# Kernel optimization log

Measured on AMD Instinct MI355X. Metric: run time of the kernel, lower is better.

Reference implementation:

```python
import jax, jax.numpy as jnp
import numpy as np
from jax import lax

P = 4
PSIZE = P * P
ITERS = 3
EPS = 1e-8
LAMBDA = 1e-3  # inverse-temperature used by the EM routing sigmoid (yl-1993 style)
LN2PI_HALF = 0.5 * float(np.log(2.0 * np.pi))


def extract_patches(x, K, stride, pad):
    """x: (b,h,w,c) -> (b,oh,ow,K*K,c) sliding-window patches."""
    if pad:
        x = jnp.pad(x, ((0, 0), (pad, pad), (pad, pad), (0, 0)))
    b, h, w, c = x.shape
    oh = (h - K) // stride + 1
    ow = (w - K) // stride + 1
    slices = []
    for ki in range(K):
        for kj in range(K):
            slices.append(x[:, ki:ki + stride * (oh - 1) + 1:stride,
                             kj:kj + stride * (ow - 1) + 1:stride, :])
    return jnp.stack(slices, axis=3)  # (b,oh,ow,K*K,c)


def em_routing(v, a_in, beta_u, beta_a, iters=ITERS):
    """EM routing (Hinton et al. 2018).
    v: (n, Bin, Cout, PSIZE) votes, a_in: (n, Bin, 1) input activations.
    Returns mu: (n, Cout, PSIZE), a_out: (n, Cout).
    """
    n, Bin, Cout, psize = v.shape
    r = jnp.full((n, Bin, Cout), 1.0 / Cout, dtype=v.dtype)
    mu = None
    a_out = None
    for it in range(iters):
        # ---- M step ----
        r_w = r * a_in                                    # (n,Bin,Cout)
        r_sum = r_w.sum(axis=1, keepdims=True)            # (n,1,Cout)
        coeff = (r_w / (r_sum + EPS))[..., None]          # (n,Bin,Cout,1)
        mu = jnp.sum(coeff * v, axis=1, keepdims=True)    # (n,1,Cout,psize)
        sigma_sq = jnp.sum(coeff * (v - mu) ** 2, axis=1, keepdims=True) + EPS
        cost_h = (beta_u[None, None, :, None] + 0.5 * jnp.log(sigma_sq)) * r_sum[..., None]
        a_out = jax.nn.sigmoid(LAMBDA * (beta_a[None, None, :] - cost_h.sum(axis=3)))  # (n,1,Cout)
        # ---- E step ----
        if it < iters - 1:
            ln_p = -(v - mu) ** 2 / (2.0 * sigma_sq) - 0.5 * jnp.log(sigma_sq) - LN2PI_HALF
            ln_ap = ln_p.sum(axis=3) + jnp.log(EPS + a_out)  # (n,Bin,Cout)
            r = jax.nn.softmax(ln_ap, axis=2)
    return mu[:, 0], a_out[:, 0]


def depthwise_caps(pose, a, W, bu, ba, K, stride):
    """DepthWiseConvCaps: each capsule type routes its own KxK spatial patch to one
    output capsule of the same type. W: (K*K, B, P, P)."""
    b = pose.shape[0]
    Bc = a.shape[-1]
    pad = K // 2
    pp = extract_patches(pose, K, stride, pad)  # (b,oh,ow,KK,B*PSIZE)
    ap = extract_patches(a, K, stride, pad)     # (b,oh,ow,KK,B)
    oh, ow = pp.shape[1], pp.shape[2]
    pm = pp.reshape(b, oh, ow, K * K, Bc, P, P)
    v = jnp.einsum('bhwkcij,kcjl->bhwkcil', pm, W)            # (b,oh,ow,KK,B,P,P)
    v = v.transpose(0, 1, 2, 4, 3, 5, 6).reshape(b * oh * ow * Bc, K * K, 1, PSIZE)
    a_in = ap.transpose(0, 1, 2, 4, 3).reshape(b * oh * ow * Bc, K * K, 1)
    mu, a_out = em_routing(v, a_in, bu, ba)
    return mu.reshape(b, oh, ow, Bc * PSIZE), a_out.reshape(b, oh, ow, Bc)


def conv_caps_1x1(pose, a, W, bu, ba):
    """ConvCaps with K=1, stride=1: per-position routing Bin -> Cout. W: (Bin,Cout,P,P)."""
    b, h, w, _ = pose.shape
    Bc, Cc = W.shape[0], W.shape[1]
    pm = pose.reshape(b * h * w, Bc, P, P)
    v = jnp.einsum('nbij,bcjl->nbcil', pm, W).reshape(b * h * w, Bc, Cc, PSIZE)
    a_in = a.reshape(b * h * w, Bc)[..., None]
    mu, a_out = em_routing(v, a_in, bu, ba)
    return mu.reshape(b, h, w, Cc * PSIZE), a_out.reshape(b, h, w, Cc)


def class_caps(pose, a, W, bu, ba):
    """Class ConvCaps: w_shared across positions + coordinate addition. W: (D,E,P,P)."""
    b, h, w, _ = pose.shape
    D, E = W.shape[0], W.shape[1]
    pm = pose.reshape(b, h, w, D, P, P)
    v = jnp.einsum('bhwdij,dejl->bhwdeil', pm, W).reshape(b, h, w, D, E, PSIZE)
    # coordinate addition on the first two vote components
    coord = jnp.zeros((h, w, PSIZE), v.dtype)
    coord = coord.at[:, :, 0].add(jnp.arange(h, dtype=v.dtype)[:, None] / h)
    coord = coord.at[:, :, 1].add(jnp.arange(w, dtype=v.dtype)[None, :] / w)
    v = v + coord[None, :, :, None, None, :]
    v = v.reshape(b, h * w * D, E, PSIZE)
    a_in = a.reshape(b, h * w * D, 1)
    mu, a_out = em_routing(v, a_in, bu, ba)
    return mu, a_out  # (b,E,PSIZE), (b,E)


def _forward(x, conv1_w, conv1_b, prim_pose_w, prim_pose_b, prim_a_w, prim_a_b,
             dw1_w, dw1_bu, dw1_ba, cc1_w, cc1_bu, cc1_ba,
             dw2_w, dw2_bu, dw2_ba, cc2_w, cc2_bu, cc2_ba,
             cls_w, cls_bu, cls_ba):
    # conv stem: k5 s2 valid
    y = lax.conv_general_dilated(x, conv1_w, (2, 2), 'VALID',
                                 dimension_numbers=('NHWC', 'HWIO', 'NHWC'))
    y = jax.nn.relu(y + conv1_b)
    # primary caps: 1x1 convs for pose and activation
    pose = jnp.einsum('bhwc,cd->bhwd', y, prim_pose_w) + prim_pose_b   # (b,h,w,B*PSIZE)
    a = jax.nn.sigmoid(jnp.einsum('bhwc,cd->bhwd', y, prim_a_w) + prim_a_b)  # (b,h,w,B)
    pose, a = depthwise_caps(pose, a, dw1_w, dw1_bu, dw1_ba, K=7, stride=2)
    pose, a = conv_caps_1x1(pose, a, cc1_w, cc1_bu, cc1_ba)
    pose, a = depthwise_caps(pose, a, dw2_w, dw2_bu, dw2_ba, K=5, stride=2)
    pose, a = conv_caps_1x1(pose, a, cc2_w, cc2_bu, cc2_ba)
    pose_cls, a_cls = class_caps(pose, a, cls_w, cls_bu, cls_ba)
    return a_cls  # (b, E)


def setup_inputs() -> dict:
    key = jax.random.key(0)
    ks = jax.random.split(key, 10)
    f32 = jnp.float32
    d = {}
    d['x'] = jax.random.normal(ks[0], (32, 64, 64, 1), f32)
    d['conv1_w'] = jax.random.normal(ks[1], (5, 5, 1, 64), f32) * 0.1
    d['conv1_b'] = jnp.zeros((64,), f32)
    d['prim_pose_w'] = jax.random.normal(ks[2], (64, 128), f32) * 0.1
    d['prim_pose_b'] = jnp.zeros((128,), f32)
    d['prim_a_w'] = jax.random.normal(ks[3], (64, 8), f32) * 0.1
    d['prim_a_b'] = jnp.zeros((8,), f32)
    d['dw1_w'] = jax.random.normal(ks[4], (49, 8, 4, 4), f32) * 0.25
    d['dw1_bu'] = jnp.zeros((1,), f32)
    d['dw1_ba'] = jnp.zeros((1,), f32)
    d['cc1_w'] = jax.random.normal(ks[5], (8, 16, 4, 4), f32) * 0.25
    d['cc1_bu'] = jnp.zeros((16,), f32)
    d['cc1_ba'] = jnp.zeros((16,), f32)
    d['dw2_w'] = jax.random.normal(ks[6], (25, 16, 4, 4), f32) * 0.25
    d['dw2_bu'] = jnp.zeros((1,), f32)
    d['dw2_ba'] = jnp.zeros((1,), f32)
    d['cc2_w'] = jax.random.normal(ks[7], (16, 16, 4, 4), f32) * 0.25
    d['cc2_bu'] = jnp.zeros((16,), f32)
    d['cc2_ba'] = jnp.zeros((16,), f32)
    d['cls_w'] = jax.random.normal(ks[8], (16, 10, 4, 4), f32) * 0.25
    d['cls_bu'] = jnp.zeros((10,), f32)
    d['cls_ba'] = jnp.zeros((10,), f32)
    return d


def reference(x, conv1_w, conv1_b, prim_pose_w, prim_pose_b, prim_a_w, prim_a_b,
              dw1_w, dw1_bu, dw1_ba, cc1_w, cc1_bu, cc1_ba,
              dw2_w, dw2_bu, dw2_ba, cc2_w, cc2_bu, cc2_ba,
              cls_w, cls_bu, cls_ba):
    return _forward(x, conv1_w, conv1_b, prim_pose_w, prim_pose_b, prim_a_w, prim_a_b,
                    dw1_w, dw1_bu, dw1_ba, cc1_w, cc1_bu, cc1_ba,
                    dw2_w, dw2_bu, dw2_ba, cc2_w, cc2_bu, cc2_ba,
                    cls_w, cls_bu, cls_ba)
```

## Files before the change

kernel.cpp:

```cpp
#include <hip/hip_runtime.h>
#include <hip/hip_bf16.h>

#define EPS 1e-8f
#define LAMBDA 1e-3f
#define LN2PI_HALF 0.9189385332046727f

__device__ __forceinline__ float sigmoidf(float x) { return 1.f / (1.f + __expf(-x)); }

__global__ __launch_bounds__(256) void stem_primary_kernel(
    const float* __restrict__ x, const float* __restrict__ w,
    const float* __restrict__ bias,
    const float* __restrict__ wp, const float* __restrict__ bp,
    const float* __restrict__ wa, const float* __restrict__ ba,
    float* __restrict__ pose, float* __restrict__ a) {
  __shared__ float wp_s[64][128];
  __shared__ float wc_s[25][64];
  __shared__ float wa_s[64][8];
  __shared__ float bias_s[64];
  __shared__ float bp_s[128];
  __shared__ float ba_s[8];
  __shared__ float xs[5][23];
  __shared__ float ys[10][64];

  int t = threadIdx.x;
  int jt = blockIdx.x % 3;
  int oi = (blockIdx.x / 3) % 30;
  int b  = blockIdx.x / 90;
  int oj0 = jt * 10;

  for (int q = t; q < 8192; q += 256) ((float*)wp_s)[q] = wp[q];
  for (int q = t; q < 1600; q += 256) ((float*)wc_s)[q] = w[q];
  for (int q = t; q < 512;  q += 256) ((float*)wa_s)[q] = wa[q];
  if (t < 64) bias_s[t] = bias[t];
  if (t < 128) bp_s[t] = bp[t];
  if (t < 8) ba_s[t] = ba[t];
  for (int q = t; q < 115; q += 256) {
    int ki = q / 23, kj = q % 23;
    xs[ki][kj] = x[(b * 64 + 2 * oi + ki) * 64 + 2 * oj0 + kj];
  }
  __syncthreads();

#pragma unroll
  for (int rep = 0; rep < 3; ++rep) {
    int q = rep * 256 + t;
    if (q < 640) {
      int pos = q >> 6, ch = q & 63;
      float s = bias_s[ch];
#pragma unroll
      for (int ki = 0; ki < 5; ++ki)
#pragma unroll
        for (int kj = 0; kj < 5; ++kj)
          s += xs[ki][2 * pos + kj] * wc_s[ki * 5 + kj][ch];
      ys[pos][ch] = fmaxf(s, 0.f);
    }
  }
  __syncthreads();

  int w_ = t >> 7, d = t & 127;
  float acc[5];
#pragma unroll
  for (int j = 0; j < 5; ++j) acc[j] = bp_s[d];
  for (int c = 0; c < 64; ++c) {
    float wv = wp_s[c][d];
#pragma unroll
    for (int j = 0; j < 5; ++j) acc[j] += ys[w_ + 2 * j][c] * wv;
  }
  size_t rowbase = (size_t)(b * 30 + oi) * 30 + oj0;
#pragma unroll
  for (int j = 0; j < 5; ++j)
    pose[(rowbase + w_ + 2 * j) * 128 + d] = acc[j];

  if (t < 80) {
    int pos = t >> 3, jj = t & 7;
    float s = ba_s[jj];
#pragma unroll 8
    for (int c = 0; c < 64; ++c) s += ys[pos][c] * wa_s[c][jj];
    a[(rowbase + pos) * 8 + jj] = sigmoidf(s);
  }
}

template <int K, int BC, int HIN, int WIN, int HOUT, int WOUT>
__global__ __launch_bounds__(256) void dw_caps_kernel(
    const float* __restrict__ pose_in, const float* __restrict__ a_in,
    const float* __restrict__ Wt,
    const float* __restrict__ bu_p, const float* __restrict__ ba_p,
    float* __restrict__ pose_out, float* __restrict__ a_out) {
  constexpr int PAD = K / 2;
  int tid = blockIdx.x * 256 + threadIdx.x;
  int p = tid & 15;
  int prob = tid >> 4;
  int c = prob % BC;
  int t1 = prob / BC;
  int oj = t1 % WOUT; t1 /= WOUT;
  int oi = t1 % HOUT;
  int b = t1 / HOUT;
  int ip = p >> 2, l = p & 3;

  int ih0 = 2 * oi - PAD, iw0 = 2 * oj - PAD;
  float rsum = 0.f, acc = 0.f, acc2 = 0.f;

  if (ih0 >= 0 && ih0 + K <= HIN && iw0 >= 0 && iw0 + K <= WIN) {
#pragma unroll
    for (int ki = 0; ki < K; ++ki) {
      int rowbase = (b * HIN + ih0 + ki) * WIN + iw0;
#pragma unroll
      for (int kj = 0; kj < K; ++kj) {
        int base = rowbase + kj;
        float ak = a_in[(size_t)base * BC + c];
        const float* pm = pose_in + ((size_t)base * BC + c) * 16 + ip * 4;
        const float* wr = Wt + ((ki * K + kj) * BC + c) * 16 + l;
        float v = pm[0] * wr[0] + pm[1] * wr[4] + pm[2] * wr[8] + pm[3] * wr[12];
        rsum += ak;
        float av = ak * v;
        acc += av;
        acc2 += av * v;
      }
    }
  } else {
#pragma unroll
    for (int ki = 0; ki < K; ++ki) {
      int ih = ih0 + ki;
      if (ih < 0 || ih >= HIN) continue;
      int rowbase = (b * HIN + ih) * WIN;
#pragma unroll
      for (int kj = 0; kj < K; ++kj) {
        int iw = iw0 + kj;
        if (iw < 0 || iw >= WIN) continue;
        int base = rowbase + iw;
        float ak = a_in[(size_t)base * BC + c];
        const float* pm = pose_in + ((size_t)base * BC + c) * 16 + ip * 4;
        const float* wr = Wt + ((ki * K + kj) * BC + c) * 16 + l;
        float v = pm[0] * wr[0] + pm[1] * wr[4] + pm[2] * wr[8] + pm[3] * wr[12];
        rsum += ak;
        float av = ak * v;
        acc += av;
        acc2 += av * v;
      }
    }
  }
  float inv = 1.f / (rsum + EPS);
  float mu = acc * inv;
  float S = rsum * inv;
  float sg = acc2 * inv - mu * mu * (2.f - S);
  sg = fmaxf(sg, 0.f) + EPS;
  float hl = 0.5f * __logf(sg);
  float ls = hl;
  ls += __shfl_xor(ls, 1, 64);
  ls += __shfl_xor(ls, 2, 64);
  ls += __shfl_xor(ls, 4, 64);
  ls += __shfl_xor(ls, 8, 64);

  size_t obase = ((size_t)(b * HOUT + oi) * WOUT + oj) * BC + c;
  pose_out[obase * 16 + p] = mu;
  if (p == 0) {
    float cost = rsum * (16.f * bu_p[0] + ls);
    a_out[obase] = sigmoidf(LAMBDA * (ba_p[0] - cost));
  }
}

template <int BIN>
__global__ __launch_bounds__(256) void cc_em_kernel(
    const float* __restrict__ pose_in, const float* __restrict__ a_arr,
    const float* __restrict__ Wt,
    const float* __restrict__ bu_p, const float* __restrict__ ba_p,
    float* __restrict__ pose_out, float* __restrict__ a_out) {
  constexpr int COUT = 16;
  __shared__ float pm_s[BIN * 16];
  __shared__ float ain_s[BIN];
  __shared__ float v_s[BIN][COUT * 16];
  __shared__ float rw_s[BIN][COUT];
  __shared__ float mu_s[COUT * 16];
  __shared__ float sg_s[COUT * 16];
  __shared__ float hl_s[COUT * 16];
  __shared__ float rsum_s[COUT];
  __shared__ float aout_s[COUT];
  __shared__ float lnap_s[BIN][COUT];

  int n = blockIdx.x, t = threadIdx.x;
  int c = t >> 4, p = t & 15;
  if (t < BIN * 16) pm_s[t] = pose_in[(size_t)n * BIN * 16 + t];
  if (t < BIN) ain_s[t] = a_arr[(size_t)n * BIN + t];
  __syncthreads();

  int ip = p >> 2, l = p & 3;
#pragma unroll
  for (int b = 0; b < BIN; ++b) {
    const float* wr = Wt + (b * COUT + c) * 16 + l;
    const float* pm = &pm_s[b * 16 + ip * 4];
    v_s[b][t] = pm[0] * wr[0] + pm[1] * wr[4] + pm[2] * wr[8] + pm[3] * wr[12];
  }
  if (t < BIN * COUT) rw_s[t / COUT][t % COUT] = (1.f / COUT) * ain_s[t / COUT];
  __syncthreads();

  for (int it = 0; it < 3; ++it) {
    if (t < COUT) {
      float s = 0.f;
#pragma unroll
      for (int b = 0; b < BIN; ++b) s += rw_s[b][t];
      rsum_s[t] = s;
    }
    __syncthreads();
    {
      float s = 0.f;
#pragma unroll
      for (int b = 0; b < BIN; ++b) s += rw_s[b][c] * v_s[b][t];
      float mu = s / (rsum_s[c] + EPS);
      mu_s[t] = mu;
      float s2 = 0.f;
#pragma unroll
      for (int b = 0; b < BIN; ++b) { float d = v_s[b][t] - mu; s2 += rw_s[b][c] * d * d; }
      float sg = s2 / (rsum_s[c] + EPS) + EPS;
      sg_s[t] = sg;
      hl_s[t] = 0.5f * __logf(sg);
    }
    __syncthreads();
    if (t < COUT) {
      float lsum = 0.f;
#pragma unroll
      for (int pp = 0; pp < 16; ++pp) lsum += hl_s[t * 16 + pp];
      float cost = rsum_s[t] * (16.f * bu_p[t] + lsum);
      aout_s[t] = sigmoidf(LAMBDA * (ba_p[t] - cost));
    }
    __syncthreads();
    if (it < 2) {
      if (t < BIN * COUT) {
        int b = t / COUT, cc = t % COUT;
        float s = __logf(EPS + aout_s[cc]) - 16.f * LN2PI_HALF;
#pragma unroll
        for (int pp = 0; pp < 16; ++pp) {
          float d = v_s[b][cc * 16 + pp] - mu_s[cc * 16 + pp];
          s += -d * d / (2.f * sg_s[cc * 16 + pp]) - hl_s[cc * 16 + pp];
        }
        lnap_s[b][cc] = s;
      }
      __syncthreads();
      if (t < BIN * COUT) {
        int b = t / COUT, cc = t % COUT;
        float m = -1e30f;
#pragma unroll
        for (int q = 0; q < COUT; ++q) m = fmaxf(m, lnap_s[b][q]);
        float Z = 0.f;
#pragma unroll
        for (int q = 0; q < COUT; ++q) Z += __expf(lnap_s[b][q] - m);
        rw_s[b][cc] = (__expf(lnap_s[b][cc] - m) / Z) * ain_s[b];
      }
      __syncthreads();
    }
  }
  pose_out[(size_t)n * COUT * 16 + t] = mu_s[t];
  if (t < COUT) a_out[(size_t)n * COUT + t] = aout_s[t];
}

__global__ __launch_bounds__(256) void cls_m_kernel(
    const float* __restrict__ pose5, const float* __restrict__ a5,
    const float* __restrict__ X, const float* __restrict__ W,
    const float* __restrict__ bu_p, const float* __restrict__ ba_p,
    float* __restrict__ mu_g, float* __restrict__ inv2_g,
    float* __restrict__ base_g, float* __restrict__ out,
    int first, int last) {
  int blk = blockIdx.x;
  int c = blk % 10, b = blk / 10;
  int t = threadIdx.x;
  int lane = t & 63, wv = t >> 6;
  const float* pg = pose5 + (size_t)b * 16384;
  __shared__ float w_s[16][16];
  {
    int d = t & 15, jj = t >> 4;
    w_s[jj][d] = W[(d * 10 + c) * 16 + jj];
  }
  __syncthreads();
  const int d = t & 15;
  float wf[16];
#pragma unroll
  for (int jj = 0; jj < 16; ++jj) wf[jj] = w_s[jj][d];

  float sA = 0.f, sV[16], sV2[16];
#pragma unroll
  for (int p = 0; p < 16; ++p) { sV[p] = 0.f; sV2[p] = 0.f; }
#pragma unroll
  for (int rep = 0; rep < 4; ++rep) {
    int bi = rep * 256 + t;
    int pos = bi >> 4;
    float rw = first ? 0.1f * a5[(size_t)b * 1024 + bi]
                     : X[(size_t)blk * 1024 + bi];
    float ci = (float)(pos >> 3) * 0.125f;
    float cj = (float)(pos & 7) * 0.125f;
    const float* pp = pg + pos * 256 + d * 16;
    float pmr[16];
#pragma unroll
    for (int q = 0; q < 16; ++q) pmr[q] = pp[q];
    sA += rw;
#pragma unroll
    for (int p = 0; p < 16; ++p) {
      int ip = p >> 2, l = p & 3;
      float v = pmr[ip * 4 + 0] * wf[0 * 4 + l] + pmr[ip * 4 + 1] * wf[1 * 4 + l]
              + pmr[ip * 4 + 2] * wf[2 * 4 + l] + pmr[ip * 4 + 3] * wf[3 * 4 + l];
      if (p == 0) v += ci;
      else if (p == 1) v += cj;
      float rv = rw * v;
      sV[p] += rv;
      sV2[p] += rv * v;
    }
  }
#pragma unroll
  for (int off = 1; off < 64; off <<= 1) {
    sA += __shfl_xor(sA, off, 64);
#pragma unroll
    for (int p = 0; p < 16; ++p) {
      sV[p]  += __shfl_xor(sV[p],  off, 64);
      sV2[p] += __shfl_xor(sV2[p], off, 64);
    }
  }
  __shared__ float red[4][36];
  if (lane == 0) {
    red[wv][0] = sA;
#pragma unroll
    for (int p = 0; p < 16; ++p) { red[wv][1 + p] = sV[p]; red[wv][17 + p] = sV2[p]; }
  }
  __syncthreads();
  if (t < 16) {
    int p = t;
    float sAf  = red[0][0] + red[1][0] + red[2][0] + red[3][0];
    float sVf  = red[0][1+p] + red[1][1+p] + red[2][1+p] + red[3][1+p];
    float sV2f = red[0][17+p] + red[1][17+p] + red[2][17+p] + red[3][17+p];
    float inv = 1.f / (sAf + EPS);
    float S = sAf * inv;
    float mu = sVf * inv;
    float sg = sV2f * inv - mu * mu * (2.f - S) + EPS;
    sg = fmaxf(sg, EPS);
    mu_g[blk * 16 + p] = mu;
    inv2_g[blk * 16 + p] = 0.5f / sg;
    float hl = 0.5f * __logf(sg);
    float lsum = hl;
    lsum += __shfl_xor(lsum, 1, 64);
    lsum += __shfl_xor(lsum, 2, 64);
    lsum += __shfl_xor(lsum, 4, 64);
    lsum += __shfl_xor(lsum, 8, 64);
    if (p == 0) {
      float cost = sAf * (16.f * bu_p[c] + lsum);
      float ao = sigmoidf(LAMBDA * (ba_p[c] - cost));
      base_g[blk] = __logf(EPS + ao) - lsum - 16.f * LN2PI_HALF;
      if (last) out[blk] = ao;
    }
  }
}

__global__ __launch_bounds__(512) void cls_e_kernel(
    const float* __restrict__ pose5, const float* __restrict__ a5,
    const float* __restrict__ W,
    const float* __restrict__ mu_g, const float* __restrict__ inv2_g,
    const float* __restrict__ base_g, float* __restrict__ X) {
  int b = blockIdx.x >> 1;
  int t = threadIdx.x;
  int bi = ((blockIdx.x & 1) << 9) + t;
  const float* pg = pose5 + (size_t)b * 16384;
  __shared__ float w2[10][16][16];
  __shared__ float mu_s[160];
  __shared__ float inv2_s[160];
  __shared__ float base_s[10];
  for (int q = t; q < 2560; q += 512) {
    int dd = q & 15, jj = (q >> 4) & 15, c = q >> 8;
    w2[c][jj][dd] = W[(dd * 10 + c) * 16 + jj];
  }
  if (t < 160) { mu_s[t] = mu_g[b * 160 + t]; inv2_s[t] = inv2_g[b * 160 + t]; }
  if (t >= 160 && t < 170) base_s[t - 160] = base_g[b * 10 + (t - 160)];
  __syncthreads();

  int pos = bi >> 4, d2 = bi & 15;
  float ci = (float)(pos >> 3) * 0.125f;
  float cj = (float)(pos & 7) * 0.125f;
  const float* pp = pg + pos * 256 + d2 * 16;
  float pmr[16];
#pragma unroll
  for (int q = 0; q < 16; ++q) pmr[q] = pp[q];
  float lnap[10];
#pragma unroll
  for (int c = 0; c < 10; ++c) {
    float wf[16];
#pragma unroll
    for (int jj = 0; jj < 16; ++jj) wf[jj] = w2[c][jj][d2];
    float s = base_s[c];
#pragma unroll
    for (int p = 0; p < 16; ++p) {
      int ip = p >> 2, l = p & 3;
      float v = pmr[ip * 4 + 0] * wf[0 * 4 + l] + pmr[ip * 4 + 1] * wf[1 * 4 + l]
              + pmr[ip * 4 + 2] * wf[2 * 4 + l] + pmr[ip * 4 + 3] * wf[3 * 4 + l];
      if (p == 0) v += ci;
      else if (p == 1) v += cj;
      float dd = v - mu_s[c * 16 + p];
      s -= dd * dd * inv2_s[c * 16 + p];
    }
    lnap[c] = s;
  }
  float m = -1e30f;
#pragma unroll
  for (int c = 0; c < 10; ++c) m = fmaxf(m, lnap[c]);
  float Z = 0.f;
  float ex[10];
#pragma unroll
  for (int c = 0; c < 10; ++c) { ex[c] = __expf(lnap[c] - m); Z += ex[c]; }
  float invZ = a5[(size_t)b * 1024 + bi] / Z;
#pragma unroll
  for (int c = 0; c < 10; ++c) X[((size_t)(b * 10 + c)) * 1024 + bi] = ex[c] * invZ;
}

extern "C" void kernel_launch(void* const* d_in, const int* in_sizes, int n_in,
                              void* d_out, int out_size, void* d_ws, size_t ws_size,
                              hipStream_t stream) {
  const float* x       = (const float*)d_in[0];
  const float* conv1_w = (const float*)d_in[1];
  const float* conv1_b = (const float*)d_in[2];
  const float* pp_w    = (const float*)d_in[3];
  const float* pp_b    = (const float*)d_in[4];
  const float* pa_w    = (const float*)d_in[5];
  const float* pa_b    = (const float*)d_in[6];
  const float* dw1_w   = (const float*)d_in[7];
  const float* dw1_bu  = (const float*)d_in[8];
  const float* dw1_ba  = (const float*)d_in[9];
  const float* cc1_w   = (const float*)d_in[10];
  const float* cc1_bu  = (const float*)d_in[11];
  const float* cc1_ba  = (const float*)d_in[12];
  const float* dw2_w   = (const float*)d_in[13];
  const float* dw2_bu  = (const float*)d_in[14];
  const float* dw2_ba  = (const float*)d_in[15];
  const float* cc2_w   = (const float*)d_in[16];
  const float* cc2_bu  = (const float*)d_in[17];
  const float* cc2_ba  = (const float*)d_in[18];
  const float* cls_w   = (const float*)d_in[19];
  const float* cls_bu  = (const float*)d_in[20];
  const float* cls_ba  = (const float*)d_in[21];
  float* out = (float*)d_out;

  float* ws = (float*)d_ws;
  float* pose1 = ws;
  float* a1    = ws + 3686400;
  float* pose2 = ws + 3916800;
  float* a2    = ws + 4838400;
  float* pose3 = ws;
  float* a3    = ws + 1843200;
  float* pose4 = ws + 1958400;
  float* a4    = ws + 2482688;
  float* pose5 = ws + 2515456;
  float* a5    = ws + 3039744;
  float* Xbuf  = ws + 3072512;
  float* mu_g  = ws + 3400192;
  float* inv2_g= ws + 3405312;
  float* base_g= ws + 3410432;

  stem_primary_kernel<<<2880, 256, 0, stream>>>(x, conv1_w, conv1_b,
                                                pp_w, pp_b, pa_w, pa_b, pose1, a1);
  dw_caps_kernel<7, 8, 30, 30, 15, 15><<<3600, 256, 0, stream>>>(
      pose1, a1, dw1_w, dw1_bu, dw1_ba, pose2, a2);
  cc_em_kernel<8><<<7200, 256, 0, stream>>>(pose2, a2, cc1_w, cc1_bu, cc1_ba, pose3, a3);
  dw_caps_kernel<5, 16, 15, 15, 8, 8><<<2048, 256, 0, stream>>>(
      pose3, a3, dw2_w, dw2_bu, dw2_ba, pose4, a4);
  cc_em_kernel<16><<<2048, 256, 0, stream>>>(pose4, a4, cc2_w, cc2_bu, cc2_ba, pose5, a5);
  cls_m_kernel<<<320, 256, 0, stream>>>(pose5, a5, Xbuf, cls_w, cls_bu, cls_ba,
                                        mu_g, inv2_g, base_g, out, 1, 0);
  cls_e_kernel<<<64, 512, 0, stream>>>(pose5, a5, cls_w, mu_g, inv2_g, base_g, Xbuf);
  cls_m_kernel<<<320, 256, 0, stream>>>(pose5, a5, Xbuf, cls_w, cls_bu, cls_ba,
                                        mu_g, inv2_g, base_g, out, 0, 0);
  cls_e_kernel<<<64, 512, 0, stream>>>(pose5, a5, cls_w, mu_g, inv2_g, base_g, Xbuf);
  cls_m_kernel<<<320, 256, 0, stream>>>(pose5, a5, Xbuf, cls_w, cls_bu, cls_ba,
                                        mu_g, inv2_g, base_g, out, 0, 1);
}
```

Measured before the change: 302.8 us.

## Stage depthwise capsule input rows and weights in shared memory per block

```diff
diff --git a/kernel.cpp b/kernel.cpp
--- a/kernel.cpp
+++ b/kernel.cpp
@@ -79,82 +79,88 @@
   }
 }
 
-template <int K, int BC, int HIN, int WIN, int HOUT, int WOUT>
+template <int K, int BC, int HIN, int WIN, int HOUT, int WOUT, int OIG, int NG>
 __global__ __launch_bounds__(256) void dw_caps_kernel(
     const float* __restrict__ pose_in, const float* __restrict__ a_in,
     const float* __restrict__ Wt,
     const float* __restrict__ bu_p, const float* __restrict__ ba_p,
     float* __restrict__ pose_out, float* __restrict__ a_out) {
   constexpr int PAD = K / 2;
-  int tid = blockIdx.x * 256 + threadIdx.x;
-  int p = tid & 15;
-  int prob = tid >> 4;
-  int c = prob % BC;
-  int t1 = prob / BC;
-  int oj = t1 % WOUT; t1 /= WOUT;
-  int oi = t1 % HOUT;
-  int b = t1 / HOUT;
-  int ip = p >> 2, l = p & 3;
-
-  int ih0 = 2 * oi - PAD, iw0 = 2 * oj - PAD;
-  float rsum = 0.f, acc = 0.f, acc2 = 0.f;
-
-  if (ih0 >= 0 && ih0 + K <= HIN && iw0 >= 0 && iw0 + K <= WIN) {
+  constexpr int RA = (2 * (OIG - 1) + K < HIN) ? (2 * (OIG - 1) + K) : HIN;
+  __shared__ float tp[RA * WIN * 20];
+  __shared__ float ta[RA * WIN];
+  __shared__ float wt[K * K * 16];
+
+  int t = threadIdx.x;
+  int g = (NG > 1) ? (blockIdx.x % NG) : 0;
+  int c = (blockIdx.x / NG) % BC;
+  int b = blockIdx.x / (NG * BC);
+  int oi_lo = g * OIG;
+  int rlo = max(0, 2 * oi_lo - PAD);
+  int rhi = min(HIN, 2 * (oi_lo + OIG - 1) - PAD + K);
+  int nrows = rhi - rlo;
+
+  for (int q = t; q < K * K * 16; q += 256) {
+    int tap = q >> 4, lj = q & 15, l = lj >> 2, j = lj & 3;
+    wt[tap * 16 + lj] = Wt[((size_t)tap * BC + c) * 16 + j * 4 + l];
+  }
+  for (int q = t; q < nrows * WIN; q += 256) {
+    int row = q / WIN, col = q % WIN;
+    ta[q] = a_in[((size_t)((b * HIN + rlo + row) * WIN + col)) * BC + c];
+  }
+  for (int q = t; q < nrows * WIN * 4; q += 256) {
+    int quad = q & 3, pc = q >> 2;
+    int row = pc / WIN, col = pc % WIN;
+    const float4 src = *(const float4*)(pose_in +
+        (((size_t)((b * HIN + rlo + row) * WIN + col)) * BC + c) * 16 + quad * 4);
+    *(float4*)(tp + (row * WIN + col) * 20 + quad * 4) = src;
+  }
+  __syncthreads();
+
+  for (int s = t; s < OIG * WOUT * 16; s += 256) {
+    int p = s & 15, pr = s >> 4;
+    int oj = pr % WOUT;
+    int oi = oi_lo + pr / WOUT;
+    int ip = p >> 2, l = p & 3;
+    int ih0 = 2 * oi - PAD, iw0 = 2 * oj - PAD;
+    float rsum = 0.f, acc = 0.f, acc2 = 0.f;
 #pragma unroll
     for (int ki = 0; ki < K; ++ki) {
-      int rowbase = (b * HIN + ih0 + ki) * WIN + iw0;
+      int ih = ih0 + ki;
+      if (ih < 0 || ih >= HIN) continue;
+      int rbase = (ih - rlo) * WIN;
 #pragma unroll
       for (int kj = 0; kj < K; ++kj) {
-        int base = rowbase + kj;
-        float ak = a_in[(size_t)base * BC + c];
-        const float* pm = pose_in + ((size_t)base * BC + c) * 16 + ip * 4;
-        const float* wr = Wt + ((ki * K + kj) * BC + c) * 16 + l;
-        float v = pm[0] * wr[0] + pm[1] * wr[4] + pm[2] * wr[8] + pm[3] * wr[12];
+        int iw = iw0 + kj;
+        if (iw < 0 || iw >= WIN) continue;
+        float ak = ta[rbase + iw];
+        const float4 pm = *(const float4*)(tp + (rbase + iw) * 20 + ip * 4);
+        const float4 wr = *(const float4*)(wt + (ki * K + kj) * 16 + l * 4);
+        float v = pm.x * wr.x + pm.y * wr.y + pm.z * wr.z + pm.w * wr.w;
         rsum += ak;
         float av = ak * v;
         acc += av;
         acc2 += av * v;
       }
     }
-  } else {
-#pragma unroll
-    for (int ki = 0; ki < K; ++ki) {
-      int ih = ih0 + ki;
-      if (ih < 0 || ih >= HIN) continue;
-      int rowbase = (b * HIN + ih) * WIN;
-#pragma unroll
-      for (int kj = 0; kj < K; ++kj) {
-        int iw = iw0 + kj;
-        if (iw < 0 || iw >= WIN) continue;
-        int base = rowbase + iw;
-        float ak = a_in[(size_t)base * BC + c];
-        const float* pm = pose_in + ((size_t)base * BC + c) * 16 + ip * 4;
-        const float* wr = Wt + ((ki * K + kj) * BC + c) * 16 + l;
-        float v = pm[0] * wr[0] + pm[1] * wr[4] + pm[2] * wr[8] + pm[3] * wr[12];
-        rsum += ak;
-        float av = ak * v;
-        acc += av;
-        acc2 += av * v;
-      }
-    }
-  }
-  float inv = 1.f / (rsum + EPS);
-  float mu = acc * inv;
-  float S = rsum * inv;
-  float sg = acc2 * inv - mu * mu * (2.f - S);
-  sg = fmaxf(sg, 0.f) + EPS;
-  float hl = 0.5f * __logf(sg);
-  float ls = hl;
-  ls += __shfl_xor(ls, 1, 64);
-  ls += __shfl_xor(ls, 2, 64);
-  ls += __shfl_xor(ls, 4, 64);
-  ls += __shfl_xor(ls, 8, 64);
-
-  size_t obase = ((size_t)(b * HOUT + oi) * WOUT + oj) * BC + c;
-  pose_out[obase * 16 + p] = mu;
-  if (p == 0) {
-    float cost = rsum * (16.f * bu_p[0] + ls);
-    a_out[obase] = sigmoidf(LAMBDA * (ba_p[0] - cost));
+    float inv = 1.f / (rsum + EPS);
+    float mu = acc * inv;
+    float S = rsum * inv;
+    float sg = acc2 * inv - mu * mu * (2.f - S);
+    sg = fmaxf(sg, 0.f) + EPS;
+    float hl = 0.5f * __logf(sg);
+    float ls = hl;
+    ls += __shfl_xor(ls, 1, 64);
+    ls += __shfl_xor(ls, 2, 64);
+    ls += __shfl_xor(ls, 4, 64);
+    ls += __shfl_xor(ls, 8, 64);
+
+    size_t obase = ((size_t)(b * HOUT + oi) * WOUT + oj) * BC + c;
+    pose_out[obase * 16 + p] = mu;
+    if (p == 0) {
+      float cost = rsum * (16.f * bu_p[0] + ls);
+      a_out[obase] = sigmoidf(LAMBDA * (ba_p[0] - cost));
+    }
   }
 }
 
@@ -449,10 +455,10 @@
 
   stem_primary_kernel<<<2880, 256, 0, stream>>>(x, conv1_w, conv1_b,
                                                 pp_w, pp_b, pa_w, pa_b, pose1, a1);
-  dw_caps_kernel<7, 8, 30, 30, 15, 15><<<3600, 256, 0, stream>>>(
+  dw_caps_kernel<7, 8, 30, 30, 15, 15, 5, 3><<<768, 256, 0, stream>>>(
       pose1, a1, dw1_w, dw1_bu, dw1_ba, pose2, a2);
   cc_em_kernel<8><<<7200, 256, 0, stream>>>(pose2, a2, cc1_w, cc1_bu, cc1_ba, pose3, a3);
-  dw_caps_kernel<5, 16, 15, 15, 8, 8><<<2048, 256, 0, stream>>>(
+  dw_caps_kernel<5, 16, 15, 15, 8, 8, 8, 1><<<512, 256, 0, stream>>>(
       pose3, a3, dw2_w, dw2_bu, dw2_ba, pose4, a4);
   cc_em_kernel<16><<<2048, 256, 0, stream>>>(pose4, a4, cc2_w, cc2_bu, cc2_ba, pose5, a5);
   cls_m_kernel<<<320, 256, 0, stream>>>(pose5, a5, Xbuf, cls_w, cls_bu, cls_ba,
```

Measured after the change: 286.2 us. -5.5%, faster.
